# Performance work log

Hardware: AMD Instinct MI355X
Metric: run time of the kernel (lower is better)

Reference implementation:

```python
import jax, jax.numpy as jnp
import numpy as np
from jax import lax

PROB_THRESHOLD = 0.9
IOU_THRESHOLD = 0.5
H, W = 80, 80


def setup_inputs() -> dict:
    key = jax.random.key(0)
    # [5, H, W]: channel 0 = probability, channels 1:5 = (x1, y1, w, h)
    x = jax.random.uniform(key, (5, H, W), dtype=jnp.float32)
    return {"x": x}


def _pairwise_iou(boxes):
    # boxes: [N, 4] in xyxy format (torchvision box_iou semantics, no +1)
    area = jnp.maximum(boxes[:, 2] - boxes[:, 0], 0.0) * jnp.maximum(boxes[:, 3] - boxes[:, 1], 0.0)
    lt = jnp.maximum(boxes[:, None, :2], boxes[None, :, :2])  # [N, N, 2]
    rb = jnp.minimum(boxes[:, None, 2:], boxes[None, :, 2:])  # [N, N, 2]
    wh = jnp.maximum(rb - lt, 0.0)
    inter = wh[..., 0] * wh[..., 1]                           # [N, N]
    union = area[:, None] + area[None, :] - inter
    return inter / jnp.maximum(union, 1e-9)


def reference(x):
    # Flatten grid: rows = [prob, x1, y1, w, h]
    flat = x.reshape(5, -1).T  # [N, 5]
    valid = flat[:, 0] > PROB_THRESHOLD

    # Faithful in-place transform from the torch code:
    #   bbx[:, 2] = bbx[:, 0] + bbx[:, 2];  bbx[:, 3] = bbx[:, 1] + bbx[:, 3]
    # (column 0 is the probability channel, exactly as the source does it)
    c2 = flat[:, 0] + flat[:, 2]
    c3 = flat[:, 1] + flat[:, 3]
    b5 = jnp.stack([flat[:, 0], flat[:, 1], c2, c3, flat[:, 4]], axis=1)  # [N, 5]

    # Sort by score descending; invalid rows pushed to the end with -inf
    scores = jnp.where(valid, b5[:, 0], -jnp.inf)
    order = jnp.argsort(-scores)
    b5_sorted = b5[order]          # [N, 5]
    valid_sorted = valid[order]    # [N]
    boxes = b5_sorted[:, 1:]       # [N, 4] -> nms(boxes=x[:,1:], scores=x[:,0])

    iou = _pairwise_iou(boxes)     # [N, N], dominant 164 MB intermediate
    N = boxes.shape[0]

    # Greedy NMS in score order: keep box i iff it is valid and no already-kept
    # higher-scoring box overlaps it with IoU > threshold.
    def body(i, keep):
        suppressed = jnp.any(keep & (iou[i] > IOU_THRESHOLD))
        return keep.at[i].set(valid_sorted[i] & ~suppressed)

    keep = lax.fori_loop(0, N, body, jnp.zeros((N,), dtype=bool))

    # Fixed-shape, jit-friendly equivalent of x[bbxis]: kept rows (score-sorted),
    # suppressed / below-threshold rows zeroed out.
    return jnp.where(keep[:, None], b5_sorted, 0.0)
```

## Files before the change

kernel.cpp:

```cpp
#include <hip/hip_runtime.h>


#define MAXM  256
#define CHUNK 200

__global__ void k_zero(float* __restrict__ out, int out_n,
                       int* __restrict__ ranks, int n, int* __restrict__ cnt) {
  int tid = blockIdx.x * blockDim.x + threadIdx.x;
  int nt = gridDim.x * blockDim.x;
  float4* o4 = (float4*)out;
  int n4 = out_n >> 2;
  for (int i = tid; i < n4; i += nt) o4[i] = make_float4(0.f, 0.f, 0.f, 0.f);
  for (int i = (n4 << 2) + tid; i < out_n; i += nt) out[i] = 0.f;
  int4* r4 = (int4*)ranks;
  int rn4 = n >> 2;
  for (int i = tid; i < rn4; i += nt) r4[i] = make_int4(0, 0, 0, 0);
  for (int i = (rn4 << 2) + tid; i < n; i += nt) ranks[i] = 0;
  if (tid < 16) cnt[tid] = 0;
}

__global__ __launch_bounds__(64) void k_rank(const float* __restrict__ X,
                                             int* __restrict__ ranks, int n) {
  int i = blockIdx.x * 64 + threadIdx.x;
  int c0 = blockIdx.y * CHUNK;
  int cend = min(c0 + CHUNK, n);
  float si = (i < n) ? X[i] : -1.f;
  bool valid = (i < n) && (si > 0.9f);
  int gt = 0, eq = 0;
  const float4* X4 = (const float4*)(X + c0);
  int nq = (cend - c0) >> 2;
  for (int q = 0; q < nq; ++q) {
    float4 v = X4[q];
    gt += (v.x > si) + (v.y > si) + (v.z > si) + (v.w > si);
    eq += (v.x == si) + (v.y == si) + (v.z == si) + (v.w == si);
  }
  for (int j = c0 + (nq << 2); j < cend; ++j) {
    float sj = X[j];
    gt += (sj > si); eq += (sj == si);
  }
  if (i >= c0 && i < cend) eq -= 1;
  int partial = gt;
  if (__any(valid && eq > 0)) {
    int eqlt = 0;
    for (int j = c0; j < cend; ++j) {
      float sj = X[j];
      eqlt += (sj == si) && (j < i);
    }
    partial = gt + eqlt;
  }
  if (valid && partial > 0) atomicAdd(&ranks[i], partial);
}

__global__ void k_rows(const float* __restrict__ X, const int* __restrict__ ranks,
                       float* __restrict__ out, float* __restrict__ list,
                       int* __restrict__ cnt, int n) {
  int i = blockIdx.x * blockDim.x + threadIdx.x;
  if (i >= n) return;
  float s = X[i];
  if (!(s > 0.9f)) return;
  int r = ranks[i];
  float f1 = X[n + i], f2 = X[2 * n + i], f3 = X[3 * n + i], f4 = X[4 * n + i];
  float c2 = s + f2, c3 = f1 + f3;
  float* row = out + (size_t)r * 5;
  row[0] = s; row[1] = f1; row[2] = c2; row[3] = c3; row[4] = f4;
  float w = fmaxf(c3 - f1, 0.f);
  float h = fmaxf(f4 - c2, 0.f);
  float area = w * h;
  if (area > 0.f) {
    int p = atomicAdd(cnt, 1);
    if (p < MAXM) {
      float* e = list + (size_t)p * 6;
      e[0] = __int_as_float(r);
      e[1] = f1; e[2] = c2; e[3] = c3; e[4] = f4; e[5] = area;
    }
  }
}

__global__ __launch_bounds__(256) void k_nms(const float* __restrict__ list,
                                             const int* __restrict__ cnt,
                                             float* __restrict__ out) {
  __shared__ int   srank[MAXM];
  __shared__ float sbox[MAXM][4];
  __shared__ float sarea[MAXM];
  __shared__ int   skeep[MAXM];
  __shared__ int   sflag;
  int t = threadIdx.x;
  int M = *cnt;
  if (M > MAXM) M = MAXM;
  for (int e = t; e < M; e += 256) {
    int r = __float_as_int(list[e * 6 + 0]);
    int pos = 0;
    for (int m = 0; m < M; ++m)
      pos += (__float_as_int(list[m * 6 + 0]) < r);
    srank[pos] = r;
    sbox[pos][0] = list[e * 6 + 1];
    sbox[pos][1] = list[e * 6 + 2];
    sbox[pos][2] = list[e * 6 + 3];
    sbox[pos][3] = list[e * 6 + 4];
    sarea[pos] = list[e * 6 + 5];
    skeep[pos] = 1;
  }
  __syncthreads();
  for (int i = 1; i < M; ++i) {
    if (t == 0) sflag = 0;
    __syncthreads();
    if (t < i && skeep[t]) {
      float ltx = fmaxf(sbox[t][0], sbox[i][0]);
      float lty = fmaxf(sbox[t][1], sbox[i][1]);
      float rbx = fminf(sbox[t][2], sbox[i][2]);
      float rby = fminf(sbox[t][3], sbox[i][3]);
      float w = fmaxf(rbx - ltx, 0.f);
      float h = fmaxf(rby - lty, 0.f);
      float inter = w * h;
      float uni = sarea[t] + sarea[i] - inter;
      if (inter / fmaxf(uni, 1e-9f) > 0.5f) sflag = 1;
    }
    __syncthreads();
    if (t == 0 && sflag) skeep[i] = 0;
    __syncthreads();
  }
  for (int e = t; e < M; e += 256) {
    if (!skeep[e]) {
      float* row = out + (size_t)srank[e] * 5;
      row[0] = 0.f; row[1] = 0.f; row[2] = 0.f; row[3] = 0.f; row[4] = 0.f;
    }
  }
}

#define FB_NTH  1024
#define FB_MAXV 2048
__global__ __launch_bounds__(FB_NTH, 1) void nms_fallback(
    const float* __restrict__ X, float* __restrict__ out, int n, int out_n) {
  __shared__ float cscore[FB_MAXV];
  __shared__ unsigned int cidx[FB_MAXV];
  __shared__ int s_vcount, s_mcount, sflag;
  __shared__ int srank[MAXM];
  __shared__ float sbox[MAXM][4];
  __shared__ float sarea[MAXM];
  __shared__ int skeep[MAXM];
  __shared__ int prank[MAXM];
  __shared__ float pbox[MAXM][4];
  __shared__ float parea[MAXM];
  const int t = threadIdx.x;
  if (t == 0) { s_vcount = 0; s_mcount = 0; }
  float4* out4 = (float4*)out;
  int n4 = out_n >> 2;
  for (int i = t; i < n4; i += FB_NTH) out4[i] = make_float4(0.f, 0.f, 0.f, 0.f);
  for (int i = (n4 << 2) + t; i < out_n; i += FB_NTH) out[i] = 0.f;
  __syncthreads();
  for (int i = t; i < n; i += FB_NTH) {
    float s = X[i];
    if (s > 0.9f) {
      int p = atomicAdd(&s_vcount, 1);
      if (p < FB_MAXV) { cscore[p] = s; cidx[p] = (unsigned int)i; }
    }
  }
  __syncthreads();
  const int V = min(s_vcount, FB_MAXV);
  for (int e = t; e < V; e += FB_NTH) {
    float s = cscore[e];
    unsigned int idx = cidx[e];
    int rank = 0;
    for (int m = 0; m < V; ++m) {
      float sm = cscore[m];
      rank += (sm > s) || (sm == s && cidx[m] < idx);
    }
    float f1 = X[n + idx], f2 = X[2 * n + idx], f3 = X[3 * n + idx], f4 = X[4 * n + idx];
    float c2 = s + f2, c3 = f1 + f3;
    float* row = out + (size_t)rank * 5;
    row[0] = s; row[1] = f1; row[2] = c2; row[3] = c3; row[4] = f4;
    float w = fmaxf(c3 - f1, 0.f), h = fmaxf(f4 - c2, 0.f);
    float area = w * h;
    if (area > 0.f) {
      int p = atomicAdd(&s_mcount, 1);
      if (p < MAXM) {
        prank[p] = rank;
        pbox[p][0] = f1; pbox[p][1] = c2; pbox[p][2] = c3; pbox[p][3] = f4;
        parea[p] = area;
      }
    }
  }
  __syncthreads();
  const int M = min(s_mcount, MAXM);
  for (int e = t; e < M; e += FB_NTH) {
    int r = prank[e];
    int pos = 0;
    for (int m = 0; m < M; ++m) pos += (prank[m] < r);
    srank[pos] = r;
    sbox[pos][0] = pbox[e][0]; sbox[pos][1] = pbox[e][1];
    sbox[pos][2] = pbox[e][2]; sbox[pos][3] = pbox[e][3];
    sarea[pos] = parea[e];
    skeep[pos] = 1;
  }
  __syncthreads();
  for (int i = 1; i < M; ++i) {
    if (t == 0) sflag = 0;
    __syncthreads();
    if (t < i && skeep[t]) {
      float ltx = fmaxf(sbox[t][0], sbox[i][0]);
      float lty = fmaxf(sbox[t][1], sbox[i][1]);
      float rbx = fminf(sbox[t][2], sbox[i][2]);
      float rby = fminf(sbox[t][3], sbox[i][3]);
      float w = fmaxf(rbx - ltx, 0.f), h = fmaxf(rby - lty, 0.f);
      float inter = w * h;
      float uni = sarea[t] + sarea[i] - inter;
      if (inter / fmaxf(uni, 1e-9f) > 0.5f) sflag = 1;
    }
    __syncthreads();
    if (t == 0 && sflag) skeep[i] = 0;
    __syncthreads();
  }
  for (int e = t; e < M; e += FB_NTH) {
    if (!skeep[e]) {
      float* row = out + (size_t)srank[e] * 5;
      row[0] = 0.f; row[1] = 0.f; row[2] = 0.f; row[3] = 0.f; row[4] = 0.f;
    }
  }
}

extern "C" void kernel_launch(void* const* d_in, const int* in_sizes, int n_in,
                              void* d_out, int out_size, void* d_ws, size_t ws_size,
                              hipStream_t stream) {
  const float* X = (const float*)d_in[0];
  float* out = (float*)d_out;
  int n = in_sizes[0] / 5;
  size_t need = 64 + (size_t)n * sizeof(int) + (size_t)MAXM * 6 * sizeof(float);
  if (ws_size >= need) {
    int* cnt = (int*)d_ws;
    int* ranks = (int*)((char*)d_ws + 64);
    float* list = (float*)((char*)d_ws + 64 + (size_t)n * sizeof(int));
    int groups = (n + 63) / 64;
    int chunks = (n + CHUNK - 1) / CHUNK;
    hipLaunchKernelGGL(k_zero, dim3(80), dim3(256), 0, stream, out, out_size, ranks, n, cnt);
    hipLaunchKernelGGL(k_rank, dim3(groups, chunks), dim3(64), 0, stream, X, ranks, n);
    hipLaunchKernelGGL(k_rows, dim3((n + 255) / 256), dim3(256), 0, stream, X, ranks, out, list, cnt, n);
    hipLaunchKernelGGL(k_nms, dim3(1), dim3(256), 0, stream, list, cnt, out);
  } else {
    hipLaunchKernelGGL(nms_fallback, dim3(1), dim3(FB_NTH), 0, stream, X, out, n, out_size);
  }
}
```

Before: 65.42 us.

## Fuse rank/rows/NMS into two kernels with partial-rank buffer and last-block NMS

Replaces the zero, rank, rows and NMS kernels with two kernels. The first writes per-chunk partial ranks for every element into a workspace buffer instead of using atomic adds, and clears the counters in one extra block. The second sums the partials, writes every output row (zeros for invalid elements, so the separate zeroing pass goes away), and a last-arriving-block pattern runs the serial NMS in the same launch. The aim is to remove launch and inter-kernel gaps; the cost is a larger workspace, a strided partial-sum read, and reliance on threadfence/atomic-load ordering for the last block.

```diff
diff --git a/kernel.cpp b/kernel.cpp
--- a/kernel.cpp
+++ b/kernel.cpp
@@ -4,28 +4,18 @@
 #define MAXM  256
 #define CHUNK 200
 
-__global__ void k_zero(float* __restrict__ out, int out_n,
-                       int* __restrict__ ranks, int n, int* __restrict__ cnt) {
-  int tid = blockIdx.x * blockDim.x + threadIdx.x;
-  int nt = gridDim.x * blockDim.x;
-  float4* o4 = (float4*)out;
-  int n4 = out_n >> 2;
-  for (int i = tid; i < n4; i += nt) o4[i] = make_float4(0.f, 0.f, 0.f, 0.f);
-  for (int i = (n4 << 2) + tid; i < out_n; i += nt) out[i] = 0.f;
-  int4* r4 = (int4*)ranks;
-  int rn4 = n >> 2;
-  for (int i = tid; i < rn4; i += nt) r4[i] = make_int4(0, 0, 0, 0);
-  for (int i = (rn4 << 2) + tid; i < n; i += nt) ranks[i] = 0;
-  if (tid < 16) cnt[tid] = 0;
-}
-
-__global__ __launch_bounds__(64) void k_rank(const float* __restrict__ X,
-                                             int* __restrict__ ranks, int n) {
-  int i = blockIdx.x * 64 + threadIdx.x;
-  int c0 = blockIdx.y * CHUNK;
-  int cend = min(c0 + CHUNK, n);
+__global__ __launch_bounds__(256) void k_rankpart(
+    const float* __restrict__ X, int* __restrict__ part,
+    int* __restrict__ counters, int n, int groups, int chunks) {
+  int b = blockIdx.x;
+  if (b >= groups * chunks) {
+    if (threadIdx.x < 8) counters[threadIdx.x] = 0;
+    return;
+  }
+  int g = b / chunks, c = b - g * chunks;
+  int i = g * 256 + threadIdx.x;
+  int c0 = c * CHUNK, cend = min(c0 + CHUNK, n);
   float si = (i < n) ? X[i] : -1.f;
-  bool valid = (i < n) && (si > 0.9f);
   int gt = 0, eq = 0;
   const float4* X4 = (const float4*)(X + c0);
   int nq = (cend - c0) >> 2;
@@ -40,83 +30,96 @@
   }
   if (i >= c0 && i < cend) eq -= 1;
   int partial = gt;
-  if (__any(valid && eq > 0)) {
+  if (__any(eq > 0)) {
     int eqlt = 0;
-    for (int j = c0; j < cend; ++j) {
-      float sj = X[j];
-      eqlt += (sj == si) && (j < i);
-    }
+    for (int j = c0; j < cend; ++j)
+      eqlt += (X[j] == si) && (j < i);
     partial = gt + eqlt;
   }
-  if (valid && partial > 0) atomicAdd(&ranks[i], partial);
-}
-
-__global__ void k_rows(const float* __restrict__ X, const int* __restrict__ ranks,
-                       float* __restrict__ out, float* __restrict__ list,
-                       int* __restrict__ cnt, int n) {
-  int i = blockIdx.x * blockDim.x + threadIdx.x;
-  if (i >= n) return;
-  float s = X[i];
-  if (!(s > 0.9f)) return;
-  int r = ranks[i];
-  float f1 = X[n + i], f2 = X[2 * n + i], f3 = X[3 * n + i], f4 = X[4 * n + i];
-  float c2 = s + f2, c3 = f1 + f3;
-  float* row = out + (size_t)r * 5;
-  row[0] = s; row[1] = f1; row[2] = c2; row[3] = c3; row[4] = f4;
-  float w = fmaxf(c3 - f1, 0.f);
-  float h = fmaxf(f4 - c2, 0.f);
-  float area = w * h;
-  if (area > 0.f) {
-    int p = atomicAdd(cnt, 1);
-    if (p < MAXM) {
-      float* e = list + (size_t)p * 6;
-      e[0] = __int_as_float(r);
-      e[1] = f1; e[2] = c2; e[3] = c3; e[4] = f4; e[5] = area;
-    }
-  }
-}
-
-__global__ __launch_bounds__(256) void k_nms(const float* __restrict__ list,
-                                             const int* __restrict__ cnt,
-                                             float* __restrict__ out) {
+  if (i < n) part[c * n + i] = partial;
+}
+
+__global__ __launch_bounds__(256) void k_finish(
+    const float* __restrict__ X, const int* __restrict__ part,
+    float* __restrict__ out, float* __restrict__ list,
+    int* __restrict__ counters, int n, int chunks, int nblocks) {
+  __shared__ int sfix;
+  const int t = threadIdx.x;
+  int i = blockIdx.x * 256 + t;
+  if (i < n) {
+    float s = X[i];
+    int r = 0;
+    for (int c = 0; c < chunks; ++c) r += part[c * n + i];
+    float* row = out + (size_t)r * 5;
+    if (s > 0.9f) {
+      float f1 = X[n + i], f2 = X[2 * n + i], f3 = X[3 * n + i], f4 = X[4 * n + i];
+      float c2 = s + f2, c3 = f1 + f3;
+      row[0] = s; row[1] = f1; row[2] = c2; row[3] = c3; row[4] = f4;
+      float w = fmaxf(c3 - f1, 0.f);
+      float h = fmaxf(f4 - c2, 0.f);
+      float area = w * h;
+      if (area > 0.f) {
+        int p = atomicAdd(&counters[0], 1);
+        if (p < MAXM) {
+          float* e = list + (size_t)p * 6;
+          e[0] = __int_as_float(r);
+          e[1] = f1; e[2] = c2; e[3] = c3; e[4] = f4; e[5] = area;
+        }
+      }
+    } else {
+      row[0] = 0.f; row[1] = 0.f; row[2] = 0.f; row[3] = 0.f; row[4] = 0.f;
+    }
+  }
+  __threadfence();
+  __syncthreads();
+  if (t == 0) {
+    int old = atomicAdd(&counters[1], 1);
+    sfix = (old == nblocks - 1);
+  }
+  __syncthreads();
+  if (!sfix) return;
+  __threadfence();
+
   __shared__ int   srank[MAXM];
   __shared__ float sbox[MAXM][4];
   __shared__ float sarea[MAXM];
   __shared__ int   skeep[MAXM];
   __shared__ int   sflag;
-  int t = threadIdx.x;
-  int M = *cnt;
+  int M = __hip_atomic_load(&counters[0], __ATOMIC_ACQUIRE, __HIP_MEMORY_SCOPE_AGENT);
   if (M > MAXM) M = MAXM;
   for (int e = t; e < M; e += 256) {
-    int r = __float_as_int(list[e * 6 + 0]);
+    float v0 = __hip_atomic_load(&list[e * 6 + 0], __ATOMIC_RELAXED, __HIP_MEMORY_SCOPE_AGENT);
+    int r = __float_as_int(v0);
     int pos = 0;
-    for (int m = 0; m < M; ++m)
-      pos += (__float_as_int(list[m * 6 + 0]) < r);
+    for (int m = 0; m < M; ++m) {
+      float vm = __hip_atomic_load(&list[m * 6 + 0], __ATOMIC_RELAXED, __HIP_MEMORY_SCOPE_AGENT);
+      pos += (__float_as_int(vm) < r);
+    }
     srank[pos] = r;
-    sbox[pos][0] = list[e * 6 + 1];
-    sbox[pos][1] = list[e * 6 + 2];
-    sbox[pos][2] = list[e * 6 + 3];
-    sbox[pos][3] = list[e * 6 + 4];
-    sarea[pos] = list[e * 6 + 5];
+    sbox[pos][0] = __hip_atomic_load(&list[e * 6 + 1], __ATOMIC_RELAXED, __HIP_MEMORY_SCOPE_AGENT);
+    sbox[pos][1] = __hip_atomic_load(&list[e * 6 + 2], __ATOMIC_RELAXED, __HIP_MEMORY_SCOPE_AGENT);
+    sbox[pos][2] = __hip_atomic_load(&list[e * 6 + 3], __ATOMIC_RELAXED, __HIP_MEMORY_SCOPE_AGENT);
+    sbox[pos][3] = __hip_atomic_load(&list[e * 6 + 4], __ATOMIC_RELAXED, __HIP_MEMORY_SCOPE_AGENT);
+    sarea[pos]   = __hip_atomic_load(&list[e * 6 + 5], __ATOMIC_RELAXED, __HIP_MEMORY_SCOPE_AGENT);
     skeep[pos] = 1;
   }
   __syncthreads();
-  for (int i = 1; i < M; ++i) {
+  for (int s = 1; s < M; ++s) {
     if (t == 0) sflag = 0;
     __syncthreads();
-    if (t < i && skeep[t]) {
-      float ltx = fmaxf(sbox[t][0], sbox[i][0]);
-      float lty = fmaxf(sbox[t][1], sbox[i][1]);
-      float rbx = fminf(sbox[t][2], sbox[i][2]);
-      float rby = fminf(sbox[t][3], sbox[i][3]);
+    if (t < s && skeep[t]) {
+      float ltx = fmaxf(sbox[t][0], sbox[s][0]);
+      float lty = fmaxf(sbox[t][1], sbox[s][1]);
+      float rbx = fminf(sbox[t][2], sbox[s][2]);
+      float rby = fminf(sbox[t][3], sbox[s][3]);
       float w = fmaxf(rbx - ltx, 0.f);
       float h = fmaxf(rby - lty, 0.f);
       float inter = w * h;
-      float uni = sarea[t] + sarea[i] - inter;
+      float uni = sarea[t] + sarea[s] - inter;
       if (inter / fmaxf(uni, 1e-9f) > 0.5f) sflag = 1;
     }
     __syncthreads();
-    if (t == 0 && sflag) skeep[i] = 0;
+    if (t == 0 && sflag) skeep[s] = 0;
     __syncthreads();
   }
   for (int e = t; e < M; e += 256) {
@@ -193,21 +196,21 @@
     skeep[pos] = 1;
   }
   __syncthreads();
-  for (int i = 1; i < M; ++i) {
+  for (int s = 1; s < M; ++s) {
     if (t == 0) sflag = 0;
     __syncthreads();
-    if (t < i && skeep[t]) {
-      float ltx = fmaxf(sbox[t][0], sbox[i][0]);
-      float lty = fmaxf(sbox[t][1], sbox[i][1]);
-      float rbx = fminf(sbox[t][2], sbox[i][2]);
-      float rby = fminf(sbox[t][3], sbox[i][3]);
+    if (t < s && skeep[t]) {
+      float ltx = fmaxf(sbox[t][0], sbox[s][0]);
+      float lty = fmaxf(sbox[t][1], sbox[s][1]);
+      float rbx = fminf(sbox[t][2], sbox[s][2]);
+      float rby = fminf(sbox[t][3], sbox[s][3]);
       float w = fmaxf(rbx - ltx, 0.f), h = fmaxf(rby - lty, 0.f);
       float inter = w * h;
-      float uni = sarea[t] + sarea[i] - inter;
+      float uni = sarea[t] + sarea[s] - inter;
       if (inter / fmaxf(uni, 1e-9f) > 0.5f) sflag = 1;
     }
     __syncthreads();
-    if (t == 0 && sflag) skeep[i] = 0;
+    if (t == 0 && sflag) skeep[s] = 0;
     __syncthreads();
   }
   for (int e = t; e < M; e += FB_NTH) {
@@ -224,17 +227,18 @@
   const float* X = (const float*)d_in[0];
   float* out = (float*)d_out;
   int n = in_sizes[0] / 5;
-  size_t need = 64 + (size_t)n * sizeof(int) + (size_t)MAXM * 6 * sizeof(float);
+  int groups = (n + 255) / 256;
+  int chunks = (n + CHUNK - 1) / CHUNK;
+  size_t part_bytes = (size_t)chunks * n * sizeof(int);
+  size_t need = 256 + part_bytes + (size_t)MAXM * 6 * sizeof(float);
   if (ws_size >= need) {
-    int* cnt = (int*)d_ws;
-    int* ranks = (int*)((char*)d_ws + 64);
-    float* list = (float*)((char*)d_ws + 64 + (size_t)n * sizeof(int));
-    int groups = (n + 63) / 64;
-    int chunks = (n + CHUNK - 1) / CHUNK;
-    hipLaunchKernelGGL(k_zero, dim3(80), dim3(256), 0, stream, out, out_size, ranks, n, cnt);
-    hipLaunchKernelGGL(k_rank, dim3(groups, chunks), dim3(64), 0, stream, X, ranks, n);
-    hipLaunchKernelGGL(k_rows, dim3((n + 255) / 256), dim3(256), 0, stream, X, ranks, out, list, cnt, n);
-    hipLaunchKernelGGL(k_nms, dim3(1), dim3(256), 0, stream, list, cnt, out);
+    int* counters = (int*)d_ws;
+    int* part = (int*)((char*)d_ws + 256);
+    float* list = (float*)((char*)d_ws + 256 + part_bytes);
+    hipLaunchKernelGGL(k_rankpart, dim3(groups * chunks + 1), dim3(256), 0, stream,
+                       X, part, counters, n, groups, chunks);
+    hipLaunchKernelGGL(k_finish, dim3(groups), dim3(256), 0, stream,
+                       X, part, out, list, counters, n, chunks, groups);
   } else {
     hipLaunchKernelGGL(nms_fallback, dim3(1), dim3(FB_NTH), 0, stream, X, out, n, out_size);
   }
```

Measured after the change: 79.31 us. 21.2% more time.

## Fuse zeroing into rank kernel and replace atomics with per-chunk partial sums

Applied to the files above, without the earlier changes.

The zeroing kernel is merged into the rank kernel as extra blocks, which removes one launch. Rank partials are now written to a per-chunk array instead of being atomically added into a zeroed rank buffer. k_rows sums the 32 chunk partials for each valid element. Rank blocks grow from 64 to 256 threads. This trades a launch and the atomics for a larger workspace buffer (chunks*n ints, about 800KB) and extra reads in k_rows.

```diff
diff --git a/kernel.cpp b/kernel.cpp
--- a/kernel.cpp
+++ b/kernel.cpp
@@ -1,34 +1,37 @@
 #include <hip/hip_runtime.h>
 
 
+#define CHUNK 200
+#define ZB    32
 #define MAXM  256
-#define CHUNK 200
-
-__global__ void k_zero(float* __restrict__ out, int out_n,
-                       int* __restrict__ ranks, int n, int* __restrict__ cnt) {
-  int tid = blockIdx.x * blockDim.x + threadIdx.x;
-  int nt = gridDim.x * blockDim.x;
-  float4* o4 = (float4*)out;
-  int n4 = out_n >> 2;
-  for (int i = tid; i < n4; i += nt) o4[i] = make_float4(0.f, 0.f, 0.f, 0.f);
-  for (int i = (n4 << 2) + tid; i < out_n; i += nt) out[i] = 0.f;
-  int4* r4 = (int4*)ranks;
-  int rn4 = n >> 2;
-  for (int i = tid; i < rn4; i += nt) r4[i] = make_int4(0, 0, 0, 0);
-  for (int i = (rn4 << 2) + tid; i < n; i += nt) ranks[i] = 0;
-  if (tid < 16) cnt[tid] = 0;
-}
-
-__global__ __launch_bounds__(64) void k_rank(const float* __restrict__ X,
-                                             int* __restrict__ ranks, int n) {
-  int i = blockIdx.x * 64 + threadIdx.x;
-  int c0 = blockIdx.y * CHUNK;
-  int cend = min(c0 + CHUNK, n);
+
+__global__ __launch_bounds__(256) void k_prep(
+    const float* __restrict__ X, int* __restrict__ part, int* __restrict__ cnt,
+    float* __restrict__ out, int out_n, int n, int chunks, int groups) {
+  const int b = blockIdx.x, t = threadIdx.x;
+  const int nrank = chunks * groups;
+
+  if (b >= nrank) {
+    int b2 = b - nrank;
+    int tid = b2 * 256 + t;
+    float4* o4 = (float4*)out;
+    int n4 = out_n >> 2;
+    for (int i = tid; i < n4; i += ZB * 256)
+      o4[i] = make_float4(0.f, 0.f, 0.f, 0.f);
+    for (int i = (n4 << 2) + tid; i < out_n; i += ZB * 256)
+      out[i] = 0.f;
+    if (b2 == 0 && t < 8) cnt[t] = 0;
+    return;
+  }
+
+  const int c = b % chunks, g = b / chunks;
+  const int i = g * 256 + t;
+  const int c0 = c * CHUNK, cend = min(c0 + CHUNK, n);
   float si = (i < n) ? X[i] : -1.f;
   bool valid = (i < n) && (si > 0.9f);
   int gt = 0, eq = 0;
   const float4* X4 = (const float4*)(X + c0);
-  int nq = (cend - c0) >> 2;
+  const int nq = (cend - c0) >> 2;
   for (int q = 0; q < nq; ++q) {
     float4 v = X4[q];
     gt += (v.x > si) + (v.y > si) + (v.z > si) + (v.w > si);
@@ -42,23 +45,23 @@
   int partial = gt;
   if (__any(valid && eq > 0)) {
     int eqlt = 0;
-    for (int j = c0; j < cend; ++j) {
-      float sj = X[j];
-      eqlt += (sj == si) && (j < i);
-    }
+    for (int j = c0; j < cend; ++j)
+      eqlt += (X[j] == si) && (j < i);
     partial = gt + eqlt;
   }
-  if (valid && partial > 0) atomicAdd(&ranks[i], partial);
-}
-
-__global__ void k_rows(const float* __restrict__ X, const int* __restrict__ ranks,
-                       float* __restrict__ out, float* __restrict__ list,
-                       int* __restrict__ cnt, int n) {
-  int i = blockIdx.x * blockDim.x + threadIdx.x;
+  if (i < n) part[c * n + i] = partial;
+}
+
+__global__ __launch_bounds__(256) void k_rows(
+    const float* __restrict__ X, const int* __restrict__ part,
+    float* __restrict__ out, float* __restrict__ list,
+    int* __restrict__ cnt, int n, int chunks) {
+  int i = blockIdx.x * 256 + threadIdx.x;
   if (i >= n) return;
   float s = X[i];
   if (!(s > 0.9f)) return;
-  int r = ranks[i];
+  int r = 0;
+  for (int c = 0; c < chunks; ++c) r += part[c * n + i];
   float f1 = X[n + i], f2 = X[2 * n + i], f3 = X[3 * n + i], f4 = X[4 * n + i];
   float c2 = s + f2, c3 = f1 + f3;
   float* row = out + (size_t)r * 5;
@@ -97,7 +100,7 @@
     sbox[pos][1] = list[e * 6 + 2];
     sbox[pos][2] = list[e * 6 + 3];
     sbox[pos][3] = list[e * 6 + 4];
-    sarea[pos] = list[e * 6 + 5];
+    sarea[pos]   = list[e * 6 + 5];
     skeep[pos] = 1;
   }
   __syncthreads();
@@ -129,18 +132,19 @@
 
 #define FB_NTH  1024
 #define FB_MAXV 2048
+#define FB_MAXM 256
 __global__ __launch_bounds__(FB_NTH, 1) void nms_fallback(
     const float* __restrict__ X, float* __restrict__ out, int n, int out_n) {
   __shared__ float cscore[FB_MAXV];
   __shared__ unsigned int cidx[FB_MAXV];
   __shared__ int s_vcount, s_mcount, sflag;
-  __shared__ int srank[MAXM];
-  __shared__ float sbox[MAXM][4];
-  __shared__ float sarea[MAXM];
-  __shared__ int skeep[MAXM];
-  __shared__ int prank[MAXM];
-  __shared__ float pbox[MAXM][4];
-  __shared__ float parea[MAXM];
+  __shared__ int srank[FB_MAXM];
+  __shared__ float sbox[FB_MAXM][4];
+  __shared__ float sarea[FB_MAXM];
+  __shared__ int skeep[FB_MAXM];
+  __shared__ int prank[FB_MAXM];
+  __shared__ float pbox[FB_MAXM][4];
+  __shared__ float parea[FB_MAXM];
   const int t = threadIdx.x;
   if (t == 0) { s_vcount = 0; s_mcount = 0; }
   float4* out4 = (float4*)out;
@@ -173,7 +177,7 @@
     float area = w * h;
     if (area > 0.f) {
       int p = atomicAdd(&s_mcount, 1);
-      if (p < MAXM) {
+      if (p < FB_MAXM) {
         prank[p] = rank;
         pbox[p][0] = f1; pbox[p][1] = c2; pbox[p][2] = c3; pbox[p][3] = f4;
         parea[p] = area;
@@ -181,7 +185,7 @@
     }
   }
   __syncthreads();
-  const int M = min(s_mcount, MAXM);
+  const int M = min(s_mcount, FB_MAXM);
   for (int e = t; e < M; e += FB_NTH) {
     int r = prank[e];
     int pos = 0;
@@ -193,21 +197,21 @@
     skeep[pos] = 1;
   }
   __syncthreads();
-  for (int i = 1; i < M; ++i) {
+  for (int s = 1; s < M; ++s) {
     if (t == 0) sflag = 0;
     __syncthreads();
-    if (t < i && skeep[t]) {
-      float ltx = fmaxf(sbox[t][0], sbox[i][0]);
-      float lty = fmaxf(sbox[t][1], sbox[i][1]);
-      float rbx = fminf(sbox[t][2], sbox[i][2]);
-      float rby = fminf(sbox[t][3], sbox[i][3]);
+    if (t < s && skeep[t]) {
+      float ltx = fmaxf(sbox[t][0], sbox[s][0]);
+      float lty = fmaxf(sbox[t][1], sbox[s][1]);
+      float rbx = fminf(sbox[t][2], sbox[s][2]);
+      float rby = fminf(sbox[t][3], sbox[s][3]);
       float w = fmaxf(rbx - ltx, 0.f), h = fmaxf(rby - lty, 0.f);
       float inter = w * h;
-      float uni = sarea[t] + sarea[i] - inter;
+      float uni = sarea[t] + sarea[s] - inter;
       if (inter / fmaxf(uni, 1e-9f) > 0.5f) sflag = 1;
     }
     __syncthreads();
-    if (t == 0 && sflag) skeep[i] = 0;
+    if (t == 0 && sflag) skeep[s] = 0;
     __syncthreads();
   }
   for (int e = t; e < M; e += FB_NTH) {
@@ -224,16 +228,19 @@
   const float* X = (const float*)d_in[0];
   float* out = (float*)d_out;
   int n = in_sizes[0] / 5;
-  size_t need = 64 + (size_t)n * sizeof(int) + (size_t)MAXM * 6 * sizeof(float);
+  int groups = (n + 255) / 256;
+  int chunks = (n + CHUNK - 1) / CHUNK;
+  size_t part_bytes = (size_t)chunks * n * sizeof(int);
+  size_t list_off = (256 + part_bytes + 15) & ~(size_t)15;
+  size_t need = list_off + (size_t)MAXM * 6 * sizeof(float);
   if (ws_size >= need) {
     int* cnt = (int*)d_ws;
-    int* ranks = (int*)((char*)d_ws + 64);
-    float* list = (float*)((char*)d_ws + 64 + (size_t)n * sizeof(int));
-    int groups = (n + 63) / 64;
-    int chunks = (n + CHUNK - 1) / CHUNK;
-    hipLaunchKernelGGL(k_zero, dim3(80), dim3(256), 0, stream, out, out_size, ranks, n, cnt);
-    hipLaunchKernelGGL(k_rank, dim3(groups, chunks), dim3(64), 0, stream, X, ranks, n);
-    hipLaunchKernelGGL(k_rows, dim3((n + 255) / 256), dim3(256), 0, stream, X, ranks, out, list, cnt, n);
+    int* part = (int*)((char*)d_ws + 256);
+    float* list = (float*)((char*)d_ws + list_off);
+    hipLaunchKernelGGL(k_prep, dim3(chunks * groups + ZB), dim3(256), 0, stream,
+                       X, part, cnt, out, out_size, n, chunks, groups);
+    hipLaunchKernelGGL(k_rows, dim3(groups), dim3(256), 0, stream,
+                       X, part, out, list, cnt, n, chunks);
     hipLaunchKernelGGL(k_nms, dim3(1), dim3(256), 0, stream, list, cnt, out);
   } else {
     hipLaunchKernelGGL(nms_fallback, dim3(1), dim3(FB_NTH), 0, stream, X, out, n, out_size);
```

Result: slower. 71.41 us (+9.1%).
